# Optimization experiments

Hardware: AMD Instinct MI355X
Metric: run time of the kernel (lower is better)

Reference implementation:

```python
import jax, jax.numpy as jnp
import numpy as np
from jax import lax

B, T, I, H = 4096, 128, 16, 64


def setup_inputs() -> dict:
    key = jax.random.key(0)
    ks = jax.random.split(key, 7)
    s_ih = 1.0 / np.sqrt(H)
    return {
        "x": jax.random.normal(ks[0], (B, T, I), dtype=jnp.float32),
        "w_ih": jax.random.uniform(ks[1], (3 * H, I), jnp.float32, -s_ih, s_ih),
        "w_hh": jax.random.uniform(ks[2], (3 * H, H), jnp.float32, -s_ih, s_ih),
        "b_ih": jax.random.uniform(ks[3], (3 * H,), jnp.float32, -s_ih, s_ih),
        "b_hh": jax.random.uniform(ks[4], (3 * H,), jnp.float32, -s_ih, s_ih),
        "fc_w": jax.random.uniform(ks[5], (1, H), jnp.float32, -s_ih, s_ih),
        "fc_b": jax.random.uniform(ks[6], (1,), jnp.float32, -s_ih, s_ih),
    }


def reference(x, w_ih, w_hh, b_ih, b_hh, fc_w, fc_b):
    # x: [B, T, I]. PyTorch GRU gate order: r, z, n.
    # Precompute input contributions to all gates for all timesteps: [B, T, 3H]
    xg = jnp.einsum('bti,gi->btg', x, w_ih) + b_ih

    def step(h, xg_t):
        # xg_t: [B, 3H], h: [B, H]
        gi_r, gi_z, gi_n = jnp.split(xg_t, 3, axis=-1)
        hg = h @ w_hh.T + b_hh  # [B, 3H]
        hr, hz, hn = jnp.split(hg, 3, axis=-1)
        r = jax.nn.sigmoid(gi_r + hr)
        z = jax.nn.sigmoid(gi_z + hz)
        n = jnp.tanh(gi_n + r * hn)
        h_new = (1.0 - z) * n + z * h
        return h_new, None

    h0 = jnp.zeros((x.shape[0], w_hh.shape[1]), dtype=x.dtype)
    hT, _ = lax.scan(step, h0, jnp.swapaxes(xg, 0, 1))  # scan over time

    # Final-step linear head, squeeze to [B]
    pred = hT @ fc_w.T + fc_b  # [B, 1]
    return pred.squeeze(-1)
```

## Files before the change

kernel.cpp:

```cpp
#include <hip/hip_runtime.h>
#include <stdint.h>


#define T_STEPS 128
#define NI 16
#define NH 64
#define RB 16
#define ROWB 272

typedef float    f32x4  __attribute__((ext_vector_type(4)));
typedef uint32_t u32x4  __attribute__((ext_vector_type(4)));
typedef uint32_t u32x2  __attribute__((ext_vector_type(2)));
typedef short    bf16x8 __attribute__((ext_vector_type(8)));
typedef __bf16   bfv8   __attribute__((ext_vector_type(8)));

static constexpr float LOG2E = 1.4426950408889634f;

static __device__ __forceinline__ uint32_t fbits(float f) { return __builtin_bit_cast(uint32_t, f); }
static __device__ __forceinline__ float    bitsf(uint32_t u) { return __builtin_bit_cast(float, u); }

static __device__ __forceinline__ bf16x8 ld_frag16(const unsigned char* p) {
  u32x4 v = *(const u32x4*)p;
  return __builtin_bit_cast(bf16x8, v);
}

#define MFMA(A, B, C) __builtin_amdgcn_mfma_f32_16x16x32_bf16(A, B, C, 0, 0, 0)

__global__ __launch_bounds__(256)
void gru_fused(const float* __restrict__ x,
               const float* __restrict__ w_ih,
               const float* __restrict__ w_hh,
               const float* __restrict__ b_ih,
               const float* __restrict__ b_hh,
               const float* __restrict__ fc_w,
               const float* __restrict__ fc_b,
               float* __restrict__ out)
{
  __shared__ __align__(16) unsigned char sH[16 * ROWB];
  __shared__ float s_red[4][16];

  const int tid  = threadIdx.x;
  const int lane = tid & 63;
  const int wv   = tid >> 6;
  const int colg = lane & 15;
  const int grp  = lane >> 4;
  const int rb   = blockIdx.x * RB;
  const int hc   = wv * 16 + colg;

  for (int i = tid; i < 1088; i += 256) ((uint32_t*)sH)[i] = 0u;

  const float scl0 = -LOG2E, scl2 = 2.0f * LOG2E;
  bf16x8 whi[3][2], wlo[3][2], axw[3];
  #pragma unroll
  for (int g = 0; g < 3; ++g) {
    const float s = (g == 2) ? scl2 : scl0;
    const float* wr = w_hh + (size_t)(g * 64 + hc) * NH + grp * 8;
    #pragma unroll
    for (int kt = 0; kt < 2; ++kt) {
      bfv8 vhi, vlo;
      #pragma unroll
      for (int j = 0; j < 8; ++j) {
        float w = wr[kt * 32 + j] * s;
        __bf16 hi = (__bf16)w;
        vhi[j] = hi;
        vlo[j] = (__bf16)(w - (float)hi);
      }
      whi[g][kt] = __builtin_bit_cast(bf16x8, vhi);
      wlo[g][kt] = __builtin_bit_cast(bf16x8, vlo);
    }
    const float* wi = w_ih + (size_t)(g * 64 + hc) * NI + (grp & 1) * 8;
    bfv8 vx;
    #pragma unroll
    for (int j = 0; j < 8; ++j) vx[j] = (__bf16)(wi[j] * s);
    axw[g] = __builtin_bit_cast(bf16x8, vx);
  }

  f32x4 bR4, bZ4, bNh4, bNx4;
  #pragma unroll
  for (int q = 0; q < 4; ++q) {
    const int hx = wv * 16 + grp * 4 + q;
    bR4[q]  = scl0 * (b_ih[hx] + b_hh[hx]);
    bZ4[q]  = scl0 * (b_ih[64 + hx] + b_hh[64 + hx]);
    bNh4[q] = scl2 * b_hh[128 + hx];
    bNx4[q] = scl2 * b_ih[128 + hx];
  }

  const int swz = colg & 7;
  const int rd_hi0 = colg * ROWB + ((0 * 4 + grp) ^ swz) * 16;
  const int rd_hi1 = colg * ROWB + ((1 * 4 + grp) ^ swz) * 16;
  const int rd_lo0 = colg * ROWB + 128 + ((0 * 4 + grp) ^ swz) * 16;
  const int rd_lo1 = colg * ROWB + 128 + ((1 * 4 + grp) ^ swz) * 16;
  const int wch   = (2 * wv + (grp >> 1)) ^ swz;
  const int wr_hi = colg * ROWB + wch * 16 + (grp & 1) * 8;
  const int wr_lo = wr_hi + 128;

  float hreg[4] = {0.f, 0.f, 0.f, 0.f};

  const float* xp = x + (size_t)(rb + colg) * T_STEPS * NI + (grp & 1) * 8;
  f32x4 xa = *(const f32x4*)(xp);
  f32x4 xb = *(const f32x4*)(xp + 4);
  const bool hi_grp = (grp < 2);

  __syncthreads();

  for (int t = 0; t < T_STEPS; ++t) {
    bf16x8 bh_hi0 = ld_frag16(sH + rd_hi0);
    bf16x8 bh_hi1 = ld_frag16(sH + rd_hi1);
    bf16x8 bh_lo0 = ld_frag16(sH + rd_lo0);
    bf16x8 bh_lo1 = ld_frag16(sH + rd_lo1);

    uint32_t d0, d1, d2, d3;
    {
      float v[8];
      #pragma unroll
      for (int j = 0; j < 4; ++j) {
        float x0 = xa[j], x1 = xb[j];
        float b0 = bitsf(fbits(x0) & 0xffff0000u);
        float b1 = bitsf(fbits(x1) & 0xffff0000u);
        v[j]     = hi_grp ? x0 : (x0 - b0);
        v[4 + j] = hi_grp ? x1 : (x1 - b1);
      }
      d0 = __builtin_amdgcn_perm(fbits(v[1]), fbits(v[0]), 0x07060302u);
      d1 = __builtin_amdgcn_perm(fbits(v[3]), fbits(v[2]), 0x07060302u);
      d2 = __builtin_amdgcn_perm(fbits(v[5]), fbits(v[4]), 0x07060302u);
      d3 = __builtin_amdgcn_perm(fbits(v[7]), fbits(v[6]), 0x07060302u);
    }
    u32x4 axu = {d0, d1, d2, d3};
    bf16x8 xfrag = __builtin_bit_cast(bf16x8, axu);

    const int tn = (t < T_STEPS - 1) ? (t + 1) : t;
    f32x4 xna = *(const f32x4*)(xp + (size_t)tn * NI);
    f32x4 xnb = *(const f32x4*)(xp + (size_t)tn * NI + 4);

    f32x4 aR  = MFMA(axw[0], xfrag, bR4);
    f32x4 aZ  = MFMA(axw[1], xfrag, bZ4);
    f32x4 aNx = MFMA(axw[2], xfrag, bNx4);

    aR = MFMA(whi[0][0], bh_hi0, aR); aR = MFMA(whi[0][1], bh_hi1, aR);
    aR = MFMA(whi[0][0], bh_lo0, aR); aR = MFMA(whi[0][1], bh_lo1, aR);
    aR = MFMA(wlo[0][0], bh_hi0, aR); aR = MFMA(wlo[0][1], bh_hi1, aR);

    aZ = MFMA(whi[1][0], bh_hi0, aZ); aZ = MFMA(whi[1][1], bh_hi1, aZ);
    aZ = MFMA(whi[1][0], bh_lo0, aZ); aZ = MFMA(whi[1][1], bh_lo1, aZ);
    aZ = MFMA(wlo[1][0], bh_hi0, aZ); aZ = MFMA(wlo[1][1], bh_hi1, aZ);

    f32x4 aNh = MFMA(whi[2][0], bh_hi0, bNh4);
    aNh = MFMA(whi[2][1], bh_hi1, aNh);
    aNh = MFMA(whi[2][0], bh_lo0, aNh); aNh = MFMA(whi[2][1], bh_lo1, aNh);
    aNh = MFMA(wlo[2][0], bh_hi0, aNh); aNh = MFMA(wlo[2][1], bh_hi1, aNh);

    float h0, h1, h2, h3;
    {
      float r = __builtin_amdgcn_rcpf(1.0f + __builtin_amdgcn_exp2f(aR[0]));
      float z = __builtin_amdgcn_rcpf(1.0f + __builtin_amdgcn_exp2f(aZ[0]));
      float n = fmaf(-2.0f, __builtin_amdgcn_rcpf(__builtin_amdgcn_exp2f(fmaf(r, aNh[0], aNx[0])) + 1.0f), 1.0f);
      h0 = n + z * (hreg[0] - n); hreg[0] = h0;
    }
    {
      float r = __builtin_amdgcn_rcpf(1.0f + __builtin_amdgcn_exp2f(aR[1]));
      float z = __builtin_amdgcn_rcpf(1.0f + __builtin_amdgcn_exp2f(aZ[1]));
      float n = fmaf(-2.0f, __builtin_amdgcn_rcpf(__builtin_amdgcn_exp2f(fmaf(r, aNh[1], aNx[1])) + 1.0f), 1.0f);
      h1 = n + z * (hreg[1] - n); hreg[1] = h1;
    }
    {
      float r = __builtin_amdgcn_rcpf(1.0f + __builtin_amdgcn_exp2f(aR[2]));
      float z = __builtin_amdgcn_rcpf(1.0f + __builtin_amdgcn_exp2f(aZ[2]));
      float n = fmaf(-2.0f, __builtin_amdgcn_rcpf(__builtin_amdgcn_exp2f(fmaf(r, aNh[2], aNx[2])) + 1.0f), 1.0f);
      h2 = n + z * (hreg[2] - n); hreg[2] = h2;
    }
    {
      float r = __builtin_amdgcn_rcpf(1.0f + __builtin_amdgcn_exp2f(aR[3]));
      float z = __builtin_amdgcn_rcpf(1.0f + __builtin_amdgcn_exp2f(aZ[3]));
      float n = fmaf(-2.0f, __builtin_amdgcn_rcpf(__builtin_amdgcn_exp2f(fmaf(r, aNh[3], aNx[3])) + 1.0f), 1.0f);
      h3 = n + z * (hreg[3] - n); hreg[3] = h3;
    }

    {
      uint32_t hi01 = __builtin_amdgcn_perm(fbits(h1), fbits(h0), 0x07060302u);
      uint32_t hi23 = __builtin_amdgcn_perm(fbits(h3), fbits(h2), 0x07060302u);
      float l0 = h0 - bitsf(fbits(h0) & 0xffff0000u);
      float l1 = h1 - bitsf(fbits(h1) & 0xffff0000u);
      float l2 = h2 - bitsf(fbits(h2) & 0xffff0000u);
      float l3 = h3 - bitsf(fbits(h3) & 0xffff0000u);
      uint32_t lo01 = __builtin_amdgcn_perm(fbits(l1), fbits(l0), 0x07060302u);
      uint32_t lo23 = __builtin_amdgcn_perm(fbits(l3), fbits(l2), 0x07060302u);
      u32x2 whiv = {hi01, hi23};
      u32x2 wlov = {lo01, lo23};
      *(u32x2*)(sH + wr_hi) = whiv;
      *(u32x2*)(sH + wr_lo) = wlov;
    }
    __syncthreads();
    xa = xna; xb = xnb;
  }

  float s;
  {
    const int hx = wv * 16 + grp * 4;
    s = hreg[0] * fc_w[hx] + hreg[1] * fc_w[hx + 1]
      + hreg[2] * fc_w[hx + 2] + hreg[3] * fc_w[hx + 3];
  }
  s += __shfl_xor(s, 16, 64);
  s += __shfl_xor(s, 32, 64);
  if (lane < 16) s_red[wv][lane] = s;
  __syncthreads();
  if (tid < 16) {
    out[rb + tid] = s_red[0][tid] + s_red[1][tid] + s_red[2][tid] + s_red[3][tid]
                  + fc_b[0];
  }
}

extern "C" void kernel_launch(void* const* d_in, const int* in_sizes, int n_in,
                              void* d_out, int out_size, void* d_ws, size_t ws_size,
                              hipStream_t stream) {
  (void)in_sizes; (void)n_in; (void)d_ws; (void)ws_size;
  const float* x    = (const float*)d_in[0];
  const float* w_ih = (const float*)d_in[1];
  const float* w_hh = (const float*)d_in[2];
  const float* b_ih = (const float*)d_in[3];
  const float* b_hh = (const float*)d_in[4];
  const float* fc_w = (const float*)d_in[5];
  const float* fc_b = (const float*)d_in[6];
  float* out = (float*)d_out;
  const int nblocks = out_size / RB;
  gru_fused<<<dim3(nblocks), dim3(256), 0, stream>>>(x, w_ih, w_hh, b_ih, b_hh,
                                                     fc_w, fc_b, out);
}
```

Baseline: 166.6 us.

## Process two independent 16-row batch tiles per block to interleave recurrences

Each block now owns 32 batch rows, split into two independent 16-row tiles with separate hidden-state buffers in shared memory. The MFMA chains and gate math of the two tiles are interleaved within each timestep, so their latencies can overlap. The bf16 packing of the next step's x is also done ahead of time, taking it off the critical path. The catch is that the grid shrinks to half as many blocks, which may leave some compute units idle, and per-thread register pressure rises.

```diff
diff --git a/kernel.cpp b/kernel.cpp
--- a/kernel.cpp
+++ b/kernel.cpp
@@ -5,8 +5,8 @@
 #define T_STEPS 128
 #define NI 16
 #define NH 64
-#define RB 16
-#define ROWB 272
+#define RB 32
+#define ROWB 288
 
 typedef float    f32x4  __attribute__((ext_vector_type(4)));
 typedef uint32_t u32x4  __attribute__((ext_vector_type(4)));
@@ -26,7 +26,53 @@
 
 #define MFMA(A, B, C) __builtin_amdgcn_mfma_f32_16x16x32_bf16(A, B, C, 0, 0, 0)
 
-__global__ __launch_bounds__(256)
+static __device__ __forceinline__ bf16x8 pack_xfrag(f32x4 xa, f32x4 xb, bool hi_grp) {
+  float v[8];
+  #pragma unroll
+  for (int j = 0; j < 4; ++j) {
+    float x0 = xa[j], x1 = xb[j];
+    float b0 = bitsf(fbits(x0) & 0xffff0000u);
+    float b1 = bitsf(fbits(x1) & 0xffff0000u);
+    v[j]     = hi_grp ? x0 : (x0 - b0);
+    v[4 + j] = hi_grp ? x1 : (x1 - b1);
+  }
+  uint32_t d0 = __builtin_amdgcn_perm(fbits(v[1]), fbits(v[0]), 0x07060302u);
+  uint32_t d1 = __builtin_amdgcn_perm(fbits(v[3]), fbits(v[2]), 0x07060302u);
+  uint32_t d2 = __builtin_amdgcn_perm(fbits(v[5]), fbits(v[4]), 0x07060302u);
+  uint32_t d3 = __builtin_amdgcn_perm(fbits(v[7]), fbits(v[6]), 0x07060302u);
+  u32x4 u = {d0, d1, d2, d3};
+  return __builtin_bit_cast(bf16x8, u);
+}
+
+static __device__ __forceinline__ void gates4(const f32x4& aR, const f32x4& aZ,
+                                              const f32x4& aNh, const f32x4& aNx,
+                                              float* hreg, unsigned char* base,
+                                              int wr_hi, int wr_lo) {
+  float h[4];
+  #pragma unroll
+  for (int q = 0; q < 4; ++q) {
+    float r = __builtin_amdgcn_rcpf(1.0f + __builtin_amdgcn_exp2f(aR[q]));
+    float z = __builtin_amdgcn_rcpf(1.0f + __builtin_amdgcn_exp2f(aZ[q]));
+    float n = fmaf(-2.0f, __builtin_amdgcn_rcpf(
+                  __builtin_amdgcn_exp2f(fmaf(r, aNh[q], aNx[q])) + 1.0f), 1.0f);
+    h[q] = n + z * (hreg[q] - n);
+    hreg[q] = h[q];
+  }
+  uint32_t hi01 = __builtin_amdgcn_perm(fbits(h[1]), fbits(h[0]), 0x07060302u);
+  uint32_t hi23 = __builtin_amdgcn_perm(fbits(h[3]), fbits(h[2]), 0x07060302u);
+  float l0 = h[0] - bitsf(fbits(h[0]) & 0xffff0000u);
+  float l1 = h[1] - bitsf(fbits(h[1]) & 0xffff0000u);
+  float l2 = h[2] - bitsf(fbits(h[2]) & 0xffff0000u);
+  float l3 = h[3] - bitsf(fbits(h[3]) & 0xffff0000u);
+  uint32_t lo01 = __builtin_amdgcn_perm(fbits(l1), fbits(l0), 0x07060302u);
+  uint32_t lo23 = __builtin_amdgcn_perm(fbits(l3), fbits(l2), 0x07060302u);
+  u32x2 whiv = {hi01, hi23};
+  u32x2 wlov = {lo01, lo23};
+  *(u32x2*)(base + wr_hi) = whiv;
+  *(u32x2*)(base + wr_lo) = wlov;
+}
+
+__global__ __launch_bounds__(256, 1)
 void gru_fused(const float* __restrict__ x,
                const float* __restrict__ w_ih,
                const float* __restrict__ w_hh,
@@ -36,8 +82,8 @@
                const float* __restrict__ fc_b,
                float* __restrict__ out)
 {
-  __shared__ __align__(16) unsigned char sH[16 * ROWB];
-  __shared__ float s_red[4][16];
+  __shared__ __align__(16) unsigned char sH[2][16 * ROWB];
+  __shared__ float s_red[2][4][16];
 
   const int tid  = threadIdx.x;
   const int lane = tid & 63;
@@ -47,7 +93,7 @@
   const int rb   = blockIdx.x * RB;
   const int hc   = wv * 16 + colg;
 
-  for (int i = tid; i < 1088; i += 256) ((uint32_t*)sH)[i] = 0u;
+  for (int i = tid; i < 2304; i += 256) ((uint32_t*)sH)[i] = 0u;
 
   const float scl0 = -LOG2E, scl2 = 2.0f * LOG2E;
   bf16x8 whi[3][2], wlo[3][2], axw[3];
@@ -88,124 +134,94 @@
   const int swz = colg & 7;
   const int rd_hi0 = colg * ROWB + ((0 * 4 + grp) ^ swz) * 16;
   const int rd_hi1 = colg * ROWB + ((1 * 4 + grp) ^ swz) * 16;
-  const int rd_lo0 = colg * ROWB + 128 + ((0 * 4 + grp) ^ swz) * 16;
-  const int rd_lo1 = colg * ROWB + 128 + ((1 * 4 + grp) ^ swz) * 16;
-  const int wch   = (2 * wv + (grp >> 1)) ^ swz;
-  const int wr_hi = colg * ROWB + wch * 16 + (grp & 1) * 8;
-  const int wr_lo = wr_hi + 128;
-
-  float hreg[4] = {0.f, 0.f, 0.f, 0.f};
-
-  const float* xp = x + (size_t)(rb + colg) * T_STEPS * NI + (grp & 1) * 8;
-  f32x4 xa = *(const f32x4*)(xp);
-  f32x4 xb = *(const f32x4*)(xp + 4);
+  const int rd_lo0 = rd_hi0 + 128;
+  const int rd_lo1 = rd_hi1 + 128;
+  const int wch    = (2 * wv + (grp >> 1)) ^ swz;
+  const int wr_hi  = colg * ROWB + wch * 16 + (grp & 1) * 8;
+  const int wr_lo  = wr_hi + 128;
+
+  float hregA[4] = {0.f, 0.f, 0.f, 0.f};
+  float hregB[4] = {0.f, 0.f, 0.f, 0.f};
+
+  const float* xpA = x + (size_t)(rb + colg) * T_STEPS * NI + (grp & 1) * 8;
+  const float* xpB = xpA + (size_t)16 * T_STEPS * NI;
   const bool hi_grp = (grp < 2);
 
+  bf16x8 xfA = pack_xfrag(*(const f32x4*)xpA, *(const f32x4*)(xpA + 4), hi_grp);
+  bf16x8 xfB = pack_xfrag(*(const f32x4*)xpB, *(const f32x4*)(xpB + 4), hi_grp);
+
   __syncthreads();
 
   for (int t = 0; t < T_STEPS; ++t) {
-    bf16x8 bh_hi0 = ld_frag16(sH + rd_hi0);
-    bf16x8 bh_hi1 = ld_frag16(sH + rd_hi1);
-    bf16x8 bh_lo0 = ld_frag16(sH + rd_lo0);
-    bf16x8 bh_lo1 = ld_frag16(sH + rd_lo1);
-
-    uint32_t d0, d1, d2, d3;
-    {
-      float v[8];
-      #pragma unroll
-      for (int j = 0; j < 4; ++j) {
-        float x0 = xa[j], x1 = xb[j];
-        float b0 = bitsf(fbits(x0) & 0xffff0000u);
-        float b1 = bitsf(fbits(x1) & 0xffff0000u);
-        v[j]     = hi_grp ? x0 : (x0 - b0);
-        v[4 + j] = hi_grp ? x1 : (x1 - b1);
-      }
-      d0 = __builtin_amdgcn_perm(fbits(v[1]), fbits(v[0]), 0x07060302u);
-      d1 = __builtin_amdgcn_perm(fbits(v[3]), fbits(v[2]), 0x07060302u);
-      d2 = __builtin_amdgcn_perm(fbits(v[5]), fbits(v[4]), 0x07060302u);
-      d3 = __builtin_amdgcn_perm(fbits(v[7]), fbits(v[6]), 0x07060302u);
-    }
-    u32x4 axu = {d0, d1, d2, d3};
-    bf16x8 xfrag = __builtin_bit_cast(bf16x8, axu);
-
     const int tn = (t < T_STEPS - 1) ? (t + 1) : t;
-    f32x4 xna = *(const f32x4*)(xp + (size_t)tn * NI);
-    f32x4 xnb = *(const f32x4*)(xp + (size_t)tn * NI + 4);
-
-    f32x4 aR  = MFMA(axw[0], xfrag, bR4);
-    f32x4 aZ  = MFMA(axw[1], xfrag, bZ4);
-    f32x4 aNx = MFMA(axw[2], xfrag, bNx4);
-
-    aR = MFMA(whi[0][0], bh_hi0, aR); aR = MFMA(whi[0][1], bh_hi1, aR);
-    aR = MFMA(whi[0][0], bh_lo0, aR); aR = MFMA(whi[0][1], bh_lo1, aR);
-    aR = MFMA(wlo[0][0], bh_hi0, aR); aR = MFMA(wlo[0][1], bh_hi1, aR);
-
-    aZ = MFMA(whi[1][0], bh_hi0, aZ); aZ = MFMA(whi[1][1], bh_hi1, aZ);
-    aZ = MFMA(whi[1][0], bh_lo0, aZ); aZ = MFMA(whi[1][1], bh_lo1, aZ);
-    aZ = MFMA(wlo[1][0], bh_hi0, aZ); aZ = MFMA(wlo[1][1], bh_hi1, aZ);
-
-    f32x4 aNh = MFMA(whi[2][0], bh_hi0, bNh4);
-    aNh = MFMA(whi[2][1], bh_hi1, aNh);
-    aNh = MFMA(whi[2][0], bh_lo0, aNh); aNh = MFMA(whi[2][1], bh_lo1, aNh);
-    aNh = MFMA(wlo[2][0], bh_hi0, aNh); aNh = MFMA(wlo[2][1], bh_hi1, aNh);
-
-    float h0, h1, h2, h3;
-    {
-      float r = __builtin_amdgcn_rcpf(1.0f + __builtin_amdgcn_exp2f(aR[0]));
-      float z = __builtin_amdgcn_rcpf(1.0f + __builtin_amdgcn_exp2f(aZ[0]));
-      float n = fmaf(-2.0f, __builtin_amdgcn_rcpf(__builtin_amdgcn_exp2f(fmaf(r, aNh[0], aNx[0])) + 1.0f), 1.0f);
-      h0 = n + z * (hreg[0] - n); hreg[0] = h0;
-    }
-    {
-      float r = __builtin_amdgcn_rcpf(1.0f + __builtin_amdgcn_exp2f(aR[1]));
-      float z = __builtin_amdgcn_rcpf(1.0f + __builtin_amdgcn_exp2f(aZ[1]));
-      float n = fmaf(-2.0f, __builtin_amdgcn_rcpf(__builtin_amdgcn_exp2f(fmaf(r, aNh[1], aNx[1])) + 1.0f), 1.0f);
-      h1 = n + z * (hreg[1] - n); hreg[1] = h1;
-    }
-    {
-      float r = __builtin_amdgcn_rcpf(1.0f + __builtin_amdgcn_exp2f(aR[2]));
-      float z = __builtin_amdgcn_rcpf(1.0f + __builtin_amdgcn_exp2f(aZ[2]));
-      float n = fmaf(-2.0f, __builtin_amdgcn_rcpf(__builtin_amdgcn_exp2f(fmaf(r, aNh[2], aNx[2])) + 1.0f), 1.0f);
-      h2 = n + z * (hreg[2] - n); hreg[2] = h2;
-    }
-    {
-      float r = __builtin_amdgcn_rcpf(1.0f + __builtin_amdgcn_exp2f(aR[3]));
-      float z = __builtin_amdgcn_rcpf(1.0f + __builtin_amdgcn_exp2f(aZ[3]));
-      float n = fmaf(-2.0f, __builtin_amdgcn_rcpf(__builtin_amdgcn_exp2f(fmaf(r, aNh[3], aNx[3])) + 1.0f), 1.0f);
-      h3 = n + z * (hreg[3] - n); hreg[3] = h3;
-    }
-
-    {
-      uint32_t hi01 = __builtin_amdgcn_perm(fbits(h1), fbits(h0), 0x07060302u);
-      uint32_t hi23 = __builtin_amdgcn_perm(fbits(h3), fbits(h2), 0x07060302u);
-      float l0 = h0 - bitsf(fbits(h0) & 0xffff0000u);
-      float l1 = h1 - bitsf(fbits(h1) & 0xffff0000u);
-      float l2 = h2 - bitsf(fbits(h2) & 0xffff0000u);
-      float l3 = h3 - bitsf(fbits(h3) & 0xffff0000u);
-      uint32_t lo01 = __builtin_amdgcn_perm(fbits(l1), fbits(l0), 0x07060302u);
-      uint32_t lo23 = __builtin_amdgcn_perm(fbits(l3), fbits(l2), 0x07060302u);
-      u32x2 whiv = {hi01, hi23};
-      u32x2 wlov = {lo01, lo23};
-      *(u32x2*)(sH + wr_hi) = whiv;
-      *(u32x2*)(sH + wr_lo) = wlov;
-    }
+    f32x4 xnaA = *(const f32x4*)(xpA + (size_t)tn * NI);
+    f32x4 xnbA = *(const f32x4*)(xpA + (size_t)tn * NI + 4);
+    f32x4 xnaB = *(const f32x4*)(xpB + (size_t)tn * NI);
+    f32x4 xnbB = *(const f32x4*)(xpB + (size_t)tn * NI + 4);
+
+    const unsigned char* bA = sH[0];
+    const unsigned char* bB = sH[1];
+    bf16x8 Ahi0 = ld_frag16(bA + rd_hi0), Ahi1 = ld_frag16(bA + rd_hi1);
+    bf16x8 Alo0 = ld_frag16(bA + rd_lo0), Alo1 = ld_frag16(bA + rd_lo1);
+    bf16x8 Bhi0 = ld_frag16(bB + rd_hi0), Bhi1 = ld_frag16(bB + rd_hi1);
+    bf16x8 Blo0 = ld_frag16(bB + rd_lo0), Blo1 = ld_frag16(bB + rd_lo1);
+
+    f32x4 aRA  = MFMA(axw[0], xfA, bR4);
+    f32x4 aZA  = MFMA(axw[1], xfA, bZ4);
+    f32x4 aNxA = MFMA(axw[2], xfA, bNx4);
+    aRA = MFMA(whi[0][0], Ahi0, aRA); aRA = MFMA(whi[0][1], Ahi1, aRA);
+    aRA = MFMA(whi[0][0], Alo0, aRA); aRA = MFMA(whi[0][1], Alo1, aRA);
+    aRA = MFMA(wlo[0][0], Ahi0, aRA); aRA = MFMA(wlo[0][1], Ahi1, aRA);
+    aZA = MFMA(whi[1][0], Ahi0, aZA); aZA = MFMA(whi[1][1], Ahi1, aZA);
+    aZA = MFMA(whi[1][0], Alo0, aZA); aZA = MFMA(whi[1][1], Alo1, aZA);
+    aZA = MFMA(wlo[1][0], Ahi0, aZA); aZA = MFMA(wlo[1][1], Ahi1, aZA);
+    f32x4 aNhA = MFMA(whi[2][0], Ahi0, bNh4);
+    aNhA = MFMA(whi[2][1], Ahi1, aNhA);
+    aNhA = MFMA(whi[2][0], Alo0, aNhA); aNhA = MFMA(whi[2][1], Alo1, aNhA);
+    aNhA = MFMA(wlo[2][0], Ahi0, aNhA); aNhA = MFMA(wlo[2][1], Ahi1, aNhA);
+
+    f32x4 aRB  = MFMA(axw[0], xfB, bR4);
+    f32x4 aZB  = MFMA(axw[1], xfB, bZ4);
+    f32x4 aNxB = MFMA(axw[2], xfB, bNx4);
+    aRB = MFMA(whi[0][0], Bhi0, aRB); aRB = MFMA(whi[0][1], Bhi1, aRB);
+    aRB = MFMA(whi[0][0], Blo0, aRB); aRB = MFMA(whi[0][1], Blo1, aRB);
+    aRB = MFMA(wlo[0][0], Bhi0, aRB); aRB = MFMA(wlo[0][1], Bhi1, aRB);
+    aZB = MFMA(whi[1][0], Bhi0, aZB); aZB = MFMA(whi[1][1], Bhi1, aZB);
+    aZB = MFMA(whi[1][0], Blo0, aZB); aZB = MFMA(whi[1][1], Blo1, aZB);
+    aZB = MFMA(wlo[1][0], Bhi0, aZB); aZB = MFMA(wlo[1][1], Bhi1, aZB);
+    f32x4 aNhB = MFMA(whi[2][0], Bhi0, bNh4);
+    aNhB = MFMA(whi[2][1], Bhi1, aNhB);
+    aNhB = MFMA(whi[2][0], Blo0, aNhB); aNhB = MFMA(whi[2][1], Blo1, aNhB);
+    aNhB = MFMA(wlo[2][0], Bhi0, aNhB); aNhB = MFMA(wlo[2][1], Bhi1, aNhB);
+
+    bf16x8 xfA_n = pack_xfrag(xnaA, xnbA, hi_grp);
+    bf16x8 xfB_n = pack_xfrag(xnaB, xnbB, hi_grp);
+
+    gates4(aRA, aZA, aNhA, aNxA, hregA, sH[0], wr_hi, wr_lo);
+    gates4(aRB, aZB, aNhB, aNxB, hregB, sH[1], wr_hi, wr_lo);
+
     __syncthreads();
-    xa = xna; xb = xnb;
-  }
-
-  float s;
+    xfA = xfA_n; xfB = xfB_n;
+  }
+
+  float sA, sB;
   {
     const int hx = wv * 16 + grp * 4;
-    s = hreg[0] * fc_w[hx] + hreg[1] * fc_w[hx + 1]
-      + hreg[2] * fc_w[hx + 2] + hreg[3] * fc_w[hx + 3];
-  }
-  s += __shfl_xor(s, 16, 64);
-  s += __shfl_xor(s, 32, 64);
-  if (lane < 16) s_red[wv][lane] = s;
+    f32x4 fw = {fc_w[hx], fc_w[hx + 1], fc_w[hx + 2], fc_w[hx + 3]};
+    sA = hregA[0] * fw[0] + hregA[1] * fw[1] + hregA[2] * fw[2] + hregA[3] * fw[3];
+    sB = hregB[0] * fw[0] + hregB[1] * fw[1] + hregB[2] * fw[2] + hregB[3] * fw[3];
+  }
+  sA += __shfl_xor(sA, 16, 64); sA += __shfl_xor(sA, 32, 64);
+  sB += __shfl_xor(sB, 16, 64); sB += __shfl_xor(sB, 32, 64);
+  if (lane < 16) {
+    s_red[0][wv][lane] = sA;
+    s_red[1][wv][lane] = sB;
+  }
   __syncthreads();
-  if (tid < 16) {
-    out[rb + tid] = s_red[0][tid] + s_red[1][tid] + s_red[2][tid] + s_red[3][tid]
-                  + fc_b[0];
+  if (tid < 32) {
+    const int g = tid >> 4, c = tid & 15;
+    out[rb + tid] = s_red[g][0][c] + s_red[g][1][c] + s_red[g][2][c]
+                  + s_red[g][3][c] + fc_b[0];
   }
 }
 
```

After: 205.4 us. 23.3% more time.

## Double-buffer hidden state in LDS and split MFMA chains for ILP

Applied to the files above, without the earlier changes.

The hidden-state staging buffer becomes double-buffered with separate hi/lo planes, so each step reads one buffer and writes the other. The dependent MFMA accumulation chains per gate are split into two independent accumulators that are summed at the end, which shortens the serial MFMA dependency. The next x fragment is now packed during the current step's gate math, and the exp2 calls are issued ahead of the reciprocals. The cost is extra LDS, a few vector adds, and more live registers.

```diff
diff --git a/kernel.cpp b/kernel.cpp
--- a/kernel.cpp
+++ b/kernel.cpp
@@ -6,7 +6,6 @@
 #define NI 16
 #define NH 64
 #define RB 16
-#define ROWB 272
 
 typedef float    f32x4  __attribute__((ext_vector_type(4)));
 typedef uint32_t u32x4  __attribute__((ext_vector_type(4)));
@@ -25,6 +24,24 @@
 }
 
 #define MFMA(A, B, C) __builtin_amdgcn_mfma_f32_16x16x32_bf16(A, B, C, 0, 0, 0)
+
+static __device__ __forceinline__ bf16x8 pack_xfrag(f32x4 xa, f32x4 xb, bool hi_grp) {
+  float v[8];
+  #pragma unroll
+  for (int j = 0; j < 4; ++j) {
+    float x0 = xa[j], x1 = xb[j];
+    float b0 = bitsf(fbits(x0) & 0xffff0000u);
+    float b1 = bitsf(fbits(x1) & 0xffff0000u);
+    v[j]     = hi_grp ? x0 : (x0 - b0);
+    v[4 + j] = hi_grp ? x1 : (x1 - b1);
+  }
+  uint32_t d0 = __builtin_amdgcn_perm(fbits(v[1]), fbits(v[0]), 0x07060302u);
+  uint32_t d1 = __builtin_amdgcn_perm(fbits(v[3]), fbits(v[2]), 0x07060302u);
+  uint32_t d2 = __builtin_amdgcn_perm(fbits(v[5]), fbits(v[4]), 0x07060302u);
+  uint32_t d3 = __builtin_amdgcn_perm(fbits(v[7]), fbits(v[6]), 0x07060302u);
+  u32x4 u = {d0, d1, d2, d3};
+  return __builtin_bit_cast(bf16x8, u);
+}
 
 __global__ __launch_bounds__(256)
 void gru_fused(const float* __restrict__ x,
@@ -36,7 +53,7 @@
                const float* __restrict__ fc_b,
                float* __restrict__ out)
 {
-  __shared__ __align__(16) unsigned char sH[16 * ROWB];
+  __shared__ __align__(16) unsigned char sH[2][2][2048];
   __shared__ float s_red[4][16];
 
   const int tid  = threadIdx.x;
@@ -47,7 +64,11 @@
   const int rb   = blockIdx.x * RB;
   const int hc   = wv * 16 + colg;
 
-  for (int i = tid; i < 1088; i += 256) ((uint32_t*)sH)[i] = 0u;
+  {
+    uint32_t* p = (uint32_t*)sH;
+    #pragma unroll
+    for (int i = 0; i < 8; ++i) p[tid + 256 * i] = 0u;
+  }
 
   const float scl0 = -LOG2E, scl2 = 2.0f * LOG2E;
   bf16x8 whi[3][2], wlo[3][2], axw[3];
@@ -86,111 +107,92 @@
   }
 
   const int swz = colg & 7;
-  const int rd_hi0 = colg * ROWB + ((0 * 4 + grp) ^ swz) * 16;
-  const int rd_hi1 = colg * ROWB + ((1 * 4 + grp) ^ swz) * 16;
-  const int rd_lo0 = colg * ROWB + 128 + ((0 * 4 + grp) ^ swz) * 16;
-  const int rd_lo1 = colg * ROWB + 128 + ((1 * 4 + grp) ^ swz) * 16;
-  const int wch   = (2 * wv + (grp >> 1)) ^ swz;
-  const int wr_hi = colg * ROWB + wch * 16 + (grp & 1) * 8;
-  const int wr_lo = wr_hi + 128;
+  const int rd0 = colg * 128 + ((0 + grp) ^ swz) * 16;
+  const int rd1 = colg * 128 + ((4 + grp) ^ swz) * 16;
+  const int wrh = colg * 128 + ((wv * 2 + (grp >> 1)) ^ swz) * 16 + (grp & 1) * 8;
 
   float hreg[4] = {0.f, 0.f, 0.f, 0.f};
 
   const float* xp = x + (size_t)(rb + colg) * T_STEPS * NI + (grp & 1) * 8;
-  f32x4 xa = *(const f32x4*)(xp);
-  f32x4 xb = *(const f32x4*)(xp + 4);
   const bool hi_grp = (grp < 2);
+  bf16x8 xf = pack_xfrag(*(const f32x4*)xp, *(const f32x4*)(xp + 4), hi_grp);
+
+  const f32x4 zz = {0.f, 0.f, 0.f, 0.f};
 
   __syncthreads();
 
   for (int t = 0; t < T_STEPS; ++t) {
-    bf16x8 bh_hi0 = ld_frag16(sH + rd_hi0);
-    bf16x8 bh_hi1 = ld_frag16(sH + rd_hi1);
-    bf16x8 bh_lo0 = ld_frag16(sH + rd_lo0);
-    bf16x8 bh_lo1 = ld_frag16(sH + rd_lo1);
-
-    uint32_t d0, d1, d2, d3;
-    {
-      float v[8];
-      #pragma unroll
-      for (int j = 0; j < 4; ++j) {
-        float x0 = xa[j], x1 = xb[j];
-        float b0 = bitsf(fbits(x0) & 0xffff0000u);
-        float b1 = bitsf(fbits(x1) & 0xffff0000u);
-        v[j]     = hi_grp ? x0 : (x0 - b0);
-        v[4 + j] = hi_grp ? x1 : (x1 - b1);
-      }
-      d0 = __builtin_amdgcn_perm(fbits(v[1]), fbits(v[0]), 0x07060302u);
-      d1 = __builtin_amdgcn_perm(fbits(v[3]), fbits(v[2]), 0x07060302u);
-      d2 = __builtin_amdgcn_perm(fbits(v[5]), fbits(v[4]), 0x07060302u);
-      d3 = __builtin_amdgcn_perm(fbits(v[7]), fbits(v[6]), 0x07060302u);
-    }
-    u32x4 axu = {d0, d1, d2, d3};
-    bf16x8 xfrag = __builtin_bit_cast(bf16x8, axu);
+    const unsigned char* rb_hi = &sH[t & 1][0][0];
+    const unsigned char* rb_lo = &sH[t & 1][1][0];
+    bf16x8 hi0 = ld_frag16(rb_hi + rd0);
+    bf16x8 hi1 = ld_frag16(rb_hi + rd1);
+    bf16x8 lo0 = ld_frag16(rb_lo + rd0);
+    bf16x8 lo1 = ld_frag16(rb_lo + rd1);
 
     const int tn = (t < T_STEPS - 1) ? (t + 1) : t;
     f32x4 xna = *(const f32x4*)(xp + (size_t)tn * NI);
     f32x4 xnb = *(const f32x4*)(xp + (size_t)tn * NI + 4);
 
-    f32x4 aR  = MFMA(axw[0], xfrag, bR4);
-    f32x4 aZ  = MFMA(axw[1], xfrag, bZ4);
-    f32x4 aNx = MFMA(axw[2], xfrag, bNx4);
-
-    aR = MFMA(whi[0][0], bh_hi0, aR); aR = MFMA(whi[0][1], bh_hi1, aR);
-    aR = MFMA(whi[0][0], bh_lo0, aR); aR = MFMA(whi[0][1], bh_lo1, aR);
-    aR = MFMA(wlo[0][0], bh_hi0, aR); aR = MFMA(wlo[0][1], bh_hi1, aR);
-
-    aZ = MFMA(whi[1][0], bh_hi0, aZ); aZ = MFMA(whi[1][1], bh_hi1, aZ);
-    aZ = MFMA(whi[1][0], bh_lo0, aZ); aZ = MFMA(whi[1][1], bh_lo1, aZ);
-    aZ = MFMA(wlo[1][0], bh_hi0, aZ); aZ = MFMA(wlo[1][1], bh_hi1, aZ);
-
-    f32x4 aNh = MFMA(whi[2][0], bh_hi0, bNh4);
-    aNh = MFMA(whi[2][1], bh_hi1, aNh);
-    aNh = MFMA(whi[2][0], bh_lo0, aNh); aNh = MFMA(whi[2][1], bh_lo1, aNh);
-    aNh = MFMA(wlo[2][0], bh_hi0, aNh); aNh = MFMA(wlo[2][1], bh_hi1, aNh);
-
-    float h0, h1, h2, h3;
+    f32x4 cR1 = MFMA(axw[0], xf, bR4);
+    f32x4 cZ1 = MFMA(axw[1], xf, bZ4);
+    f32x4 aNx = MFMA(axw[2], xf, bNx4);
+    f32x4 cR2 = MFMA(whi[0][1], lo1, zz);
+    f32x4 cZ2 = MFMA(whi[1][1], lo1, zz);
+    f32x4 cN2 = MFMA(whi[2][1], lo1, zz);
+    f32x4 cN1 = MFMA(whi[2][0], hi0, bNh4);
+    cR1 = MFMA(whi[0][0], hi0, cR1); cZ1 = MFMA(whi[1][0], hi0, cZ1);
+    cR2 = MFMA(wlo[0][0], hi0, cR2); cZ2 = MFMA(wlo[1][0], hi0, cZ2);
+    cN2 = MFMA(wlo[2][0], hi0, cN2);
+    cN1 = MFMA(whi[2][1], hi1, cN1);
+    cR1 = MFMA(whi[0][1], hi1, cR1); cZ1 = MFMA(whi[1][1], hi1, cZ1);
+    cR2 = MFMA(wlo[0][1], hi1, cR2); cZ2 = MFMA(wlo[1][1], hi1, cZ2);
+    cN2 = MFMA(wlo[2][1], hi1, cN2);
+    cN1 = MFMA(whi[2][0], lo0, cN1);
+    cR1 = MFMA(whi[0][0], lo0, cR1); cZ1 = MFMA(whi[1][0], lo0, cZ1);
+
+    f32x4 aR = cR1 + cR2;
+    f32x4 aZ = cZ1 + cZ2;
+
+    float eR0 = __builtin_amdgcn_exp2f(aR[0]), eR1 = __builtin_amdgcn_exp2f(aR[1]);
+    float eR2 = __builtin_amdgcn_exp2f(aR[2]), eR3 = __builtin_amdgcn_exp2f(aR[3]);
+    float eZ0 = __builtin_amdgcn_exp2f(aZ[0]), eZ1 = __builtin_amdgcn_exp2f(aZ[1]);
+    float eZ2 = __builtin_amdgcn_exp2f(aZ[2]), eZ3 = __builtin_amdgcn_exp2f(aZ[3]);
+
+    f32x4 aNh = cN1 + cN2;
+
+    bf16x8 xf_n = pack_xfrag(xna, xnb, hi_grp);
+
+    float eRq[4] = {eR0, eR1, eR2, eR3};
+    float eZq[4] = {eZ0, eZ1, eZ2, eZ3};
+    float h[4];
+    #pragma unroll
+    for (int q = 0; q < 4; ++q) {
+      float r = __builtin_amdgcn_rcpf(1.0f + eRq[q]);
+      float z = __builtin_amdgcn_rcpf(1.0f + eZq[q]);
+      float n = fmaf(-2.0f, __builtin_amdgcn_rcpf(
+                    __builtin_amdgcn_exp2f(fmaf(r, aNh[q], aNx[q])) + 1.0f), 1.0f);
+      h[q] = n + z * (hreg[q] - n);
+      hreg[q] = h[q];
+    }
+
     {
-      float r = __builtin_amdgcn_rcpf(1.0f + __builtin_amdgcn_exp2f(aR[0]));
-      float z = __builtin_amdgcn_rcpf(1.0f + __builtin_amdgcn_exp2f(aZ[0]));
-      float n = fmaf(-2.0f, __builtin_amdgcn_rcpf(__builtin_amdgcn_exp2f(fmaf(r, aNh[0], aNx[0])) + 1.0f), 1.0f);
-      h0 = n + z * (hreg[0] - n); hreg[0] = h0;
-    }
-    {
-      float r = __builtin_amdgcn_rcpf(1.0f + __builtin_amdgcn_exp2f(aR[1]));
-      float z = __builtin_amdgcn_rcpf(1.0f + __builtin_amdgcn_exp2f(aZ[1]));
-      float n = fmaf(-2.0f, __builtin_amdgcn_rcpf(__builtin_amdgcn_exp2f(fmaf(r, aNh[1], aNx[1])) + 1.0f), 1.0f);
-      h1 = n + z * (hreg[1] - n); hreg[1] = h1;
-    }
-    {
-      float r = __builtin_amdgcn_rcpf(1.0f + __builtin_amdgcn_exp2f(aR[2]));
-      float z = __builtin_amdgcn_rcpf(1.0f + __builtin_amdgcn_exp2f(aZ[2]));
-      float n = fmaf(-2.0f, __builtin_amdgcn_rcpf(__builtin_amdgcn_exp2f(fmaf(r, aNh[2], aNx[2])) + 1.0f), 1.0f);
-      h2 = n + z * (hreg[2] - n); hreg[2] = h2;
-    }
-    {
-      float r = __builtin_amdgcn_rcpf(1.0f + __builtin_amdgcn_exp2f(aR[3]));
-      float z = __builtin_amdgcn_rcpf(1.0f + __builtin_amdgcn_exp2f(aZ[3]));
-      float n = fmaf(-2.0f, __builtin_amdgcn_rcpf(__builtin_amdgcn_exp2f(fmaf(r, aNh[3], aNx[3])) + 1.0f), 1.0f);
-      h3 = n + z * (hreg[3] - n); hreg[3] = h3;
-    }
-
-    {
-      uint32_t hi01 = __builtin_amdgcn_perm(fbits(h1), fbits(h0), 0x07060302u);
-      uint32_t hi23 = __builtin_amdgcn_perm(fbits(h3), fbits(h2), 0x07060302u);
-      float l0 = h0 - bitsf(fbits(h0) & 0xffff0000u);
-      float l1 = h1 - bitsf(fbits(h1) & 0xffff0000u);
-      float l2 = h2 - bitsf(fbits(h2) & 0xffff0000u);
-      float l3 = h3 - bitsf(fbits(h3) & 0xffff0000u);
+      unsigned char* wb_hi = &sH[(t + 1) & 1][0][0];
+      unsigned char* wb_lo = &sH[(t + 1) & 1][1][0];
+      uint32_t hi01 = __builtin_amdgcn_perm(fbits(h[1]), fbits(h[0]), 0x07060302u);
+      uint32_t hi23 = __builtin_amdgcn_perm(fbits(h[3]), fbits(h[2]), 0x07060302u);
+      float l0 = h[0] - bitsf(fbits(h[0]) & 0xffff0000u);
+      float l1 = h[1] - bitsf(fbits(h[1]) & 0xffff0000u);
+      float l2 = h[2] - bitsf(fbits(h[2]) & 0xffff0000u);
+      float l3 = h[3] - bitsf(fbits(h[3]) & 0xffff0000u);
       uint32_t lo01 = __builtin_amdgcn_perm(fbits(l1), fbits(l0), 0x07060302u);
       uint32_t lo23 = __builtin_amdgcn_perm(fbits(l3), fbits(l2), 0x07060302u);
       u32x2 whiv = {hi01, hi23};
       u32x2 wlov = {lo01, lo23};
-      *(u32x2*)(sH + wr_hi) = whiv;
-      *(u32x2*)(sH + wr_lo) = wlov;
+      *(u32x2*)(wb_hi + wrh) = whiv;
+      *(u32x2*)(wb_lo + wrh) = wlov;
     }
     __syncthreads();
-    xa = xna; xb = xnb;
+    xf = xf_n;
   }
 
   float s;
```

Result: slower. 179.3 us (+7.6%).
